# Kernel tuning notes

Measured on AMD Instinct MI355X. Metric: run time of the kernel, lower is better.

Reference implementation:

```python
import jax, jax.numpy as jnp
import numpy as np

E = 8192       # number of edges
D = 256        # edge feature dim


def setup_inputs() -> dict:
    key = jax.random.key(0)
    ks = jax.random.split(key, 4)
    s = 1.0 / np.sqrt(D)
    return {
        "edge_x": jax.random.normal(ks[0], (E, D), dtype=jnp.float32),
        "W_sim1": jax.random.normal(ks[1], (D, D), dtype=jnp.float32) * s,
        "b_sim1": jnp.zeros((D,), dtype=jnp.float32),
        "W_sim2": jax.random.normal(ks[2], (D, D), dtype=jnp.float32) * s,
        "b_sim2": jnp.zeros((D,), dtype=jnp.float32),
        "W_out": jax.random.normal(ks[3], (3 * D, D), dtype=jnp.float32) * (1.0 / np.sqrt(3 * D)),
        "b_out": jnp.zeros((D,), dtype=jnp.float32),
    }


def reference(edge_x, W_sim1, b_sim1, W_sim2, b_sim2, W_out, b_out):
    # MPModule.forward, 'fully' branch.
    # LinearBlock = Linear + ReLU (assumed).
    e1 = jax.nn.relu(edge_x @ W_sim1 + b_sim1)            # [E, D]
    # (e1.unsqueeze(1) * e1).mean(-1)  ==  (e1 @ e1.T) / D, avoiding [E,E,D]
    sim1 = (e1 @ e1.T) / D                                 # [E, E]
    e2 = jax.nn.relu(edge_x @ W_sim2 + b_sim2)             # [E, D]
    sim2 = (e2 @ e2.T) / D                                 # [E, E]
    # (edge_x * sim.unsqueeze(-1)).sum(1) == sim @ edge_x
    agg1 = sim1 @ edge_x                                   # [E, D]
    agg2 = sim2 @ edge_x                                   # [E, D]
    h = jnp.concatenate([edge_x, agg1, agg2], axis=-1)     # [E, 3D]
    return jax.nn.relu(h @ W_out + b_out)                  # [E, D]
```

## Files before the change

### kernel.cpp

```cpp
#include <hip/hip_runtime.h>
#include <hip/hip_bf16.h>


typedef short bf16x8  __attribute__((ext_vector_type(8)));
typedef short short4v __attribute__((ext_vector_type(4)));
typedef float f32x4   __attribute__((ext_vector_type(4)));

__device__ inline short f2bf(float x) {
    unsigned u = __builtin_bit_cast(unsigned, x);
    return (short)((u + 0x7fffu + ((u >> 16) & 1u)) >> 16);
}
__device__ inline float bf2f(short b) {
    return __builtin_bit_cast(float, (unsigned)((unsigned short)b) << 16);
}
__device__ inline void cp16_async(const char* g, char* l) {
    __builtin_amdgcn_global_load_lds(
        (const __attribute__((address_space(1))) unsigned int*)g,
        (__attribute__((address_space(3))) unsigned int*)l, 16, 0, 0);
}

__global__ void prep_all(const float* __restrict__ X, short* __restrict__ h,
                         int ldh, short* __restrict__ Xt,
                         const float* __restrict__ W1, const float* __restrict__ W2,
                         const float* __restrict__ Wo,
                         short* __restrict__ Wt1, short* __restrict__ Wt2,
                         short* __restrict__ Wtoh, short* __restrict__ Bt4,
                         float* __restrict__ M)
{
    __shared__ short tile[32][33];
    const int tx = threadIdx.x, ty = threadIdx.y;
    if (blockIdx.y < 8) {
        const int r0 = blockIdx.x * 32, c0 = blockIdx.y * 32;
        #pragma unroll
        for (int i = 0; i < 4; ++i) {
            int row = ty + i * 8;
            short b = f2bf(X[(size_t)(r0 + row) * 256 + c0 + tx]);
            tile[row][tx] = b;
            int slot = ((((c0 & 32) + tx) >> 3) ^ ((r0 + row) & 7));
            h[(size_t)(r0 + row) * ldh + (c0 & ~63) + slot * 8 + (tx & 7)] = b;
        }
        __syncthreads();
        #pragma unroll
        for (int i = 0; i < 4; ++i) {
            int row = ty + i * 8;
            int d = c0 + row;
            int slot = ((((r0 & 32) + tx) >> 3) ^ (d & 7));
            Xt[(size_t)d * 8192 + (r0 & ~63) + slot * 8 + (tx & 7)] = tile[tx][row];
        }
    } else {
        int tw = (blockIdx.y - 8) * 256 + blockIdx.x;
        if (tw >= 320) {
            int i0 = (tw - 320) * 256 + ty * 32 + tx;
            for (int i = i0; i < 131072; i += 49152) M[i] = 0.f;
            return;
        }
        const float* src; short* dst; int ldwt, dk0, kx, ny;
        if (tw < 64)       { src = W1; dst = Wt1; ldwt = 256;
                             kx = tw >> 3; ny = tw & 7; dk0 = kx * 32; }
        else if (tw < 128) { int u = tw - 64; src = W2; dst = Wt2; ldwt = 256;
                             kx = u >> 3; ny = u & 7; dk0 = kx * 32; }
        else               { int u = tw - 128; int g = u >> 6; int rem = u & 63;
                             kx = rem >> 3; ny = rem & 7;
                             src = Wo + (size_t)g * 256 * 256;
                             if (g == 0) { dst = Bt4;  ldwt = 768; dk0 = kx * 32; }
                             else        { dst = Wtoh; ldwt = 512;
                                           dk0 = (g - 1) * 256 + kx * 32; } }
        const int k0l = kx * 32, n0 = ny * 32;
        #pragma unroll
        for (int i = 0; i < 4; ++i) {
            int row = ty + i * 8;
            tile[row][tx] = f2bf(src[(size_t)(k0l + row) * 256 + n0 + tx]);
        }
        __syncthreads();
        #pragma unroll
        for (int i = 0; i < 4; ++i) {
            int row = ty + i * 8;
            int n = n0 + row;
            int slot = ((((dk0 & 32) + tx) >> 3) ^ (n & 7));
            dst[(size_t)n * ldwt + (dk0 & ~63) + slot * 8 + (tx & 7)] = tile[tx][row];
        }
    }
}

__global__ __launch_bounds__(256, 1)
void gemm128(const short* __restrict__ A0, const short* __restrict__ A1, int lda,
             const short* __restrict__ B0, const short* __restrict__ B1, int ldb,
             int K,
             const float* __restrict__ bias0, const float* __restrict__ bias1,
             void* __restrict__ out0, void* __restrict__ out1,
             short* __restrict__ hout, int ldh,
             int mode, float scale)
{
    int z = blockIdx.z, sim, kbeg, kend;
    if (mode == 2) { sim = z & 1; kbeg = (z >> 1) * 512; kend = kbeg + 512; }
    else           { sim = z;     kbeg = 0;              kend = K; }
    const short* Ap   = sim ? A1 : A0;
    const short* Bp   = sim ? B1 : B0;
    const float* bias = sim ? bias1 : bias0;

    const int m0 = blockIdx.x * 128, n0 = blockIdx.y * 128;
    const int t = threadIdx.x;
    const int w = t >> 6, l = t & 63, lr = l & 15, q = l >> 4;
    const int wm = w >> 1, wn = w & 1;
    const int wub = t & ~63;

    __shared__ __attribute__((aligned(16))) short S[2][2][128 * 64];

    f32x4 acc[4][4];
    #pragma unroll
    for (int i = 0; i < 4; ++i)
        #pragma unroll
        for (int j = 0; j < 4; ++j) acc[i][j] = f32x4{0.f, 0.f, 0.f, 0.f};

    auto stage = [&](int buf, int k0) {
        #pragma unroll
        for (int it = 0; it < 4; ++it) {
            int idx = it * 256 + t;
            int r = idx >> 3, s = idx & 7;
            cp16_async((const char*)(Ap + (size_t)(m0 + r) * lda + k0) + s * 16,
                       (char*)&S[buf][0][0] + (size_t)(it * 256 + wub) * 16);
        }
        #pragma unroll
        for (int it = 0; it < 4; ++it) {
            int idx = it * 256 + t;
            int r = idx >> 3, s = idx & 7;
            cp16_async((const char*)(Bp + (size_t)(n0 + r) * ldb + k0) + s * 16,
                       (char*)&S[buf][1][0] + (size_t)(it * 256 + wub) * 16);
        }
    };

    stage(0, kbeg);
    __syncthreads();
    int cur = 0;
    for (int k0 = kbeg; k0 < kend; k0 += 64) {
        if (k0 + 64 < kend) stage(cur ^ 1, k0 + 64);
        const short* As = &S[cur][0][0];
        const short* Bs = &S[cur][1][0];
        #pragma unroll
        for (int ks = 0; ks < 2; ++ks) {
            bf16x8 af[4], bfr[4];
            #pragma unroll
            for (int mt = 0; mt < 4; ++mt) {
                int ar = wm * 64 + mt * 16 + lr;
                af[mt] = *(const bf16x8*)&As[ar * 64 + (((ks*4 + q) ^ (ar & 7)) << 3)];
            }
            #pragma unroll
            for (int nt = 0; nt < 4; ++nt) {
                int br = wn * 64 + nt * 16 + lr;
                bfr[nt] = *(const bf16x8*)&Bs[br * 64 + (((ks*4 + q) ^ (br & 7)) << 3)];
            }
            #pragma unroll
            for (int mt = 0; mt < 4; ++mt)
                #pragma unroll
                for (int nt = 0; nt < 4; ++nt)
                    acc[mt][nt] = __builtin_amdgcn_mfma_f32_16x16x32_bf16(
                        af[mt], bfr[nt], acc[mt][nt], 0, 0, 0);
        }
        __syncthreads();
        cur ^= 1;
    }

    if (mode == 0) {
        #pragma unroll
        for (int mt = 0; mt < 4; ++mt)
            #pragma unroll
            for (int nt = 0; nt < 4; ++nt)
                #pragma unroll
                for (int r = 0; r < 4; ++r) {
                    int m = m0 + wm * 64 + mt * 16 + q * 4 + r;
                    int n = n0 + wn * 64 + nt * 16 + lr;
                    float v = acc[mt][nt][r] + bias[n];
                    ((float*)out0)[(size_t)m * 256 + n] = v > 0.f ? v : 0.f;
                }
    } else if (mode == 2) {
        float* Mo = (float*)out0 + (size_t)sim * 65536;
        #pragma unroll
        for (int mt = 0; mt < 4; ++mt)
            #pragma unroll
            for (int nt = 0; nt < 4; ++nt)
                #pragma unroll
                for (int r = 0; r < 4; ++r) {
                    int m = m0 + wm * 64 + mt * 16 + q * 4 + r;
                    int n = n0 + wn * 64 + nt * 16 + lr;
                    atomicAdd(&Mo[(size_t)m * 256 + n], acc[mt][nt][r] * scale);
                }
    } else {
        short* Hs = &S[0][0][0];
        short* Ts = &S[1][0][0];
        #pragma unroll
        for (int mt = 0; mt < 4; ++mt)
            #pragma unroll
            for (int nt = 0; nt < 4; ++nt) {
                int n_loc = wn * 64 + nt * 16 + lr;
                float bb = bias[n0 + n_loc];
                short vb[4];
                #pragma unroll
                for (int r = 0; r < 4; ++r) {
                    int m_loc = wm * 64 + mt * 16 + q * 4 + r;
                    float v = acc[mt][nt][r] + bb;
                    vb[r] = f2bf(v > 0.f ? v : 0.f);
                    Hs[m_loc * 128 + n_loc] = vb[r];
                }
                int gm = wm * 8 + mt * 2 + (q >> 1);
                short4v pk = { vb[0], vb[1], vb[2], vb[3] };
                *(short4v*)&Ts[n_loc * 128 + ((gm >> 3) << 6)
                               + (((gm & 7) ^ (n_loc & 7)) << 3) + ((q & 1) << 2)] = pk;
            }
        __syncthreads();
        short* et = (short*)(sim ? out1 : out0);
        const int cb = 256 + sim * 256 + n0;
        for (int i = t; i < 2048; i += 256) {
            int ml = i >> 4, g = i & 15;
            bf16x8 hv = *(const bf16x8*)&Hs[ml * 128 + g * 8];
            *(bf16x8*)(hout + (size_t)(m0 + ml) * ldh + cb + ((g >> 3) << 6)
                       + (((g & 7) ^ (ml & 7)) << 3)) = hv;
        }
        for (int i = t; i < 2048; i += 256) {
            int nl = i >> 4, s = i & 15;
            bf16x8 tv = *(const bf16x8*)&Ts[nl * 128 + s * 8];
            *(bf16x8*)(et + (size_t)(n0 + nl) * 8192 + m0 + s * 8) = tv;
        }
    }
}

__global__ __launch_bounds__(256, 1)
void gemm_small_n(const short* __restrict__ Wtoh, const float* __restrict__ M,
                  short* __restrict__ Bt4)
{
    const int sim = blockIdx.z;
    const int n0 = blockIdx.x * 64, c0 = blockIdx.y * 64;
    const int t = threadIdx.x;
    const int w = t >> 6, l = t & 63, lr = l & 15, q = l >> 4;
    const int wub = t & ~63;
    const float* Ms = M + (size_t)sim * 65536;

    __shared__ __attribute__((aligned(16))) short As[64 * 64];
    __shared__ __attribute__((aligned(16))) short Bs[64 * 64];

    f32x4 acc[4];
    #pragma unroll
    for (int i = 0; i < 4; ++i) acc[i] = f32x4{0.f, 0.f, 0.f, 0.f};

    for (int k0 = 0; k0 < 256; k0 += 64) {
        __syncthreads();
        #pragma unroll
        for (int it = 0; it < 2; ++it) {
            int idx = it * 256 + t;
            int r = idx >> 3, s = idx & 7;
            cp16_async((const char*)(Wtoh + (size_t)(n0 + r) * 512 + sim * 256 + k0) + s * 16,
                       (char*)As + (size_t)(it * 256 + wub) * 16);
        }
        for (int i = t; i < 512; i += 256) {
            int r = i >> 3, g = i & 7;
            const float* mp = Ms + (size_t)(c0 + r) * 256 + k0 + g * 8;
            f32x4 va = *(const f32x4*)mp;
            f32x4 vb = *(const f32x4*)(mp + 4);
            bf16x8 pk;
            pk[0] = f2bf(va[0]); pk[1] = f2bf(va[1]);
            pk[2] = f2bf(va[2]); pk[3] = f2bf(va[3]);
            pk[4] = f2bf(vb[0]); pk[5] = f2bf(vb[1]);
            pk[6] = f2bf(vb[2]); pk[7] = f2bf(vb[3]);
            *(bf16x8*)&Bs[r * 64 + ((g ^ (r & 7)) << 3)] = pk;
        }
        __syncthreads();
        #pragma unroll
        for (int ks = 0; ks < 2; ++ks) {
            int arow = w * 16 + lr;
            bf16x8 af = *(const bf16x8*)&As[arow * 64 + (((ks*4 + q) ^ (arow & 7)) << 3)];
            #pragma unroll
            for (int nt = 0; nt < 4; ++nt) {
                int brow = nt * 16 + lr;
                bf16x8 bfg = *(const bf16x8*)&Bs[brow * 64 + (((ks*4 + q) ^ (brow & 7)) << 3)];
                acc[nt] = __builtin_amdgcn_mfma_f32_16x16x32_bf16(af, bfg, acc[nt], 0, 0, 0);
            }
        }
    }
    __syncthreads();
    #pragma unroll
    for (int nt = 0; nt < 4; ++nt)
        #pragma unroll
        for (int r = 0; r < 4; ++r)
            As[(w * 16 + q * 4 + r) * 64 + nt * 16 + lr] = f2bf(acc[nt][r]);
    __syncthreads();
    const int cb = 256 + sim * 256 + c0;
    for (int i = t; i < 512; i += 256) {
        int rl = i >> 3, g = i & 7;
        bf16x8 v = *(const bf16x8*)&As[rl * 64 + g * 8];
        int m = n0 + rl;
        int slot = g ^ (m & 7);
        *(bf16x8*)(Bt4 + (size_t)m * 768 + cb + slot * 8) = v;
    }
}

extern "C" void kernel_launch(void* const* d_in, const int* in_sizes, int n_in,
                              void* d_out, int out_size, void* d_ws, size_t ws_size,
                              hipStream_t stream)
{
    const float* edge_x = (const float*)d_in[0];
    const float* W1 = (const float*)d_in[1];
    const float* b1 = (const float*)d_in[2];
    const float* W2 = (const float*)d_in[3];
    const float* b2 = (const float*)d_in[4];
    const float* Wo = (const float*)d_in[5];
    const float* bo = (const float*)d_in[6];

    char* ws = (char*)d_ws;
    short* h    = (short*)ws;
    short* Xt   = (short*)(ws + 12582912);
    short* e1t  = (short*)(ws + 16777216);
    short* e2t  = (short*)(ws + 20971520);
    short* Wt1  = (short*)(ws + 25165824);
    short* Wt2  = (short*)(ws + 25296896);
    short* Wtoh = (short*)(ws + 25427968);
    short* Bt4  = (short*)(ws + 25690112);
    float* M    = (float*)(ws + 26083328);

    prep_all<<<dim3(256, 10), dim3(32, 8), 0, stream>>>(
        edge_x, h, 768, Xt, W1, W2, Wo, Wt1, Wt2, Wtoh, Bt4, M);

    gemm128<<<dim3(64, 2, 2), 256, 0, stream>>>(
        h, h, 768, Wt1, Wt2, 256, 256, b1, b2, e1t, e2t, h, 768, 1, 0.f);

    gemm128<<<dim3(2, 2, 32), 256, 0, stream>>>(
        e1t, e2t, 8192, Xt, Xt, 8192, 8192, nullptr, nullptr, M, nullptr,
        nullptr, 0, 2, 1.0f / 256.0f);

    gemm_small_n<<<dim3(4, 4, 2), 256, 0, stream>>>(Wtoh, M, Bt4);

    gemm128<<<dim3(64, 2, 1), 256, 0, stream>>>(
        h, h, 768, Bt4, Bt4, 768, 768, bo, bo, (float*)d_out, nullptr,
        nullptr, 0, 0, 0.f);
}
```

Before: 115.1 us.

## Reassociate aggregation matmuls to precompute X@Wo slices, drop X transpose

Applies associativity so that agg_i @ Wo_i = (e_i^T (X Wo_i))^T-style products are built from G_i = X @ Wo_i, computed in the first GEMM launch alongside e1/e2. The split-K E-reduction now multiplies G_i^T by e_i instead of e_i^T by X, yielding Wo-projected 256x256 matrices directly. This removes the transposed-X write in prep and the separate small GEMM, which becomes a simple fp32-to-bf16 conversion. It adds work to the first launch (four z-slices instead of two) and changes the bf16 rounding order.

```diff
diff --git a/kernel.cpp b/kernel.cpp
--- a/kernel.cpp
+++ b/kernel.cpp
@@ -20,12 +20,11 @@
 }
 
 __global__ void prep_all(const float* __restrict__ X, short* __restrict__ h,
-                         int ldh, short* __restrict__ Xt,
                          const float* __restrict__ W1, const float* __restrict__ W2,
                          const float* __restrict__ Wo,
                          short* __restrict__ Wt1, short* __restrict__ Wt2,
-                         short* __restrict__ Wtoh, short* __restrict__ Bt4,
-                         float* __restrict__ M)
+                         short* __restrict__ Wto1, short* __restrict__ Wto2,
+                         short* __restrict__ Bt4, float* __restrict__ Nacc)
 {
     __shared__ short tile[32][33];
     const int tx = threadIdx.x, ty = threadIdx.y;
@@ -35,68 +34,75 @@
         for (int i = 0; i < 4; ++i) {
             int row = ty + i * 8;
             short b = f2bf(X[(size_t)(r0 + row) * 256 + c0 + tx]);
-            tile[row][tx] = b;
             int slot = ((((c0 & 32) + tx) >> 3) ^ ((r0 + row) & 7));
-            h[(size_t)(r0 + row) * ldh + (c0 & ~63) + slot * 8 + (tx & 7)] = b;
-        }
-        __syncthreads();
-        #pragma unroll
-        for (int i = 0; i < 4; ++i) {
-            int row = ty + i * 8;
-            int d = c0 + row;
-            int slot = ((((r0 & 32) + tx) >> 3) ^ (d & 7));
-            Xt[(size_t)d * 8192 + (r0 & ~63) + slot * 8 + (tx & 7)] = tile[tx][row];
-        }
+            h[(size_t)(r0 + row) * 768 + (c0 & ~63) + slot * 8 + (tx & 7)] = b;
+        }
+        return;
+    }
+    int tw = (blockIdx.y - 8) * 256 + blockIdx.x;
+    if (tw >= 320) {
+        int i0 = (tw - 320) * 256 + ty * 32 + tx;
+        for (int i = i0; i < 131072; i += 49152) Nacc[i] = 0.f;
+        return;
+    }
+    const float* src; short* dst; int ldwt, dk0, kx, ny;
+    if (tw < 64)       { src = W1; dst = Wt1; ldwt = 256;
+                         kx = tw >> 3; ny = tw & 7; dk0 = kx * 32; }
+    else if (tw < 128) { int u = tw - 64; src = W2; dst = Wt2; ldwt = 256;
+                         kx = u >> 3; ny = u & 7; dk0 = kx * 32; }
+    else               { int u = tw - 128; int g = u >> 6; int rem = u & 63;
+                         kx = rem >> 3; ny = rem & 7;
+                         src = Wo + (size_t)g * 65536;
+                         if (g == 0) { dst = Bt4; ldwt = 768; dk0 = kx * 32; }
+                         else        { dst = (g == 1) ? Wto1 : Wto2;
+                                       ldwt = 256; dk0 = kx * 32; } }
+    const int k0l = kx * 32, n0 = ny * 32;
+    #pragma unroll
+    for (int i = 0; i < 4; ++i) {
+        int row = ty + i * 8;
+        tile[row][tx] = f2bf(src[(size_t)(k0l + row) * 256 + n0 + tx]);
+    }
+    __syncthreads();
+    #pragma unroll
+    for (int i = 0; i < 4; ++i) {
+        int row = ty + i * 8;
+        int n = n0 + row;
+        int slot = ((((dk0 & 32) + tx) >> 3) ^ (n & 7));
+        dst[(size_t)n * ldwt + (dk0 & ~63) + slot * 8 + (tx & 7)] = tile[tx][row];
+    }
+}
+
+__global__ __launch_bounds__(256, 1)
+void gemm_all(int job, short* __restrict__ h,
+              const short* __restrict__ Wt1, const short* __restrict__ Wt2,
+              const short* __restrict__ Wto1, const short* __restrict__ Wto2,
+              const short* __restrict__ Bt4,
+              const float* __restrict__ b1, const float* __restrict__ b2,
+              const float* __restrict__ bo,
+              short* __restrict__ e1t, short* __restrict__ e2t,
+              short* __restrict__ G1t, short* __restrict__ G2t,
+              float* __restrict__ Nacc, float* __restrict__ outf)
+{
+    const int z = blockIdx.z;
+    int mode, sim = 0, kbeg = 0, kend, lda, ldb;
+    const short *Ap, *Bp;
+    const float* bias = nullptr;
+    short* et = nullptr;
+    if (job == 0) {
+        Ap = h; lda = 768; kend = 256; ldb = 256;
+        if (z < 2) { mode = 1; sim = z;     Bp = z ? Wt2 : Wt1;
+                     bias = z ? b2 : b1;    et = z ? e2t : e1t; }
+        else       { mode = 3; sim = z - 2; Bp = sim ? Wto2 : Wto1;
+                     et = sim ? G2t : G1t; }
+    } else if (job == 1) {
+        mode = 2; sim = z & 1;
+        kbeg = (z >> 1) * 512; kend = kbeg + 512;
+        Ap = sim ? G2t : G1t; lda = 8192;
+        Bp = sim ? e2t : e1t; ldb = 8192;
     } else {
-        int tw = (blockIdx.y - 8) * 256 + blockIdx.x;
-        if (tw >= 320) {
-            int i0 = (tw - 320) * 256 + ty * 32 + tx;
-            for (int i = i0; i < 131072; i += 49152) M[i] = 0.f;
-            return;
-        }
-        const float* src; short* dst; int ldwt, dk0, kx, ny;
-        if (tw < 64)       { src = W1; dst = Wt1; ldwt = 256;
-                             kx = tw >> 3; ny = tw & 7; dk0 = kx * 32; }
-        else if (tw < 128) { int u = tw - 64; src = W2; dst = Wt2; ldwt = 256;
-                             kx = u >> 3; ny = u & 7; dk0 = kx * 32; }
-        else               { int u = tw - 128; int g = u >> 6; int rem = u & 63;
-                             kx = rem >> 3; ny = rem & 7;
-                             src = Wo + (size_t)g * 256 * 256;
-                             if (g == 0) { dst = Bt4;  ldwt = 768; dk0 = kx * 32; }
-                             else        { dst = Wtoh; ldwt = 512;
-                                           dk0 = (g - 1) * 256 + kx * 32; } }
-        const int k0l = kx * 32, n0 = ny * 32;
-        #pragma unroll
-        for (int i = 0; i < 4; ++i) {
-            int row = ty + i * 8;
-            tile[row][tx] = f2bf(src[(size_t)(k0l + row) * 256 + n0 + tx]);
-        }
-        __syncthreads();
-        #pragma unroll
-        for (int i = 0; i < 4; ++i) {
-            int row = ty + i * 8;
-            int n = n0 + row;
-            int slot = ((((dk0 & 32) + tx) >> 3) ^ (n & 7));
-            dst[(size_t)n * ldwt + (dk0 & ~63) + slot * 8 + (tx & 7)] = tile[tx][row];
-        }
-    }
-}
-
-__global__ __launch_bounds__(256, 1)
-void gemm128(const short* __restrict__ A0, const short* __restrict__ A1, int lda,
-             const short* __restrict__ B0, const short* __restrict__ B1, int ldb,
-             int K,
-             const float* __restrict__ bias0, const float* __restrict__ bias1,
-             void* __restrict__ out0, void* __restrict__ out1,
-             short* __restrict__ hout, int ldh,
-             int mode, float scale)
-{
-    int z = blockIdx.z, sim, kbeg, kend;
-    if (mode == 2) { sim = z & 1; kbeg = (z >> 1) * 512; kend = kbeg + 512; }
-    else           { sim = z;     kbeg = 0;              kend = K; }
-    const short* Ap   = sim ? A1 : A0;
-    const short* Bp   = sim ? B1 : B0;
-    const float* bias = sim ? bias1 : bias0;
+        mode = 0; Ap = h; lda = 768; kend = 768;
+        Bp = Bt4; ldb = 768; bias = bo;
+    }
 
     const int m0 = blockIdx.x * 128, n0 = blockIdx.y * 128;
     const int t = threadIdx.x;
@@ -170,10 +176,10 @@
                     int m = m0 + wm * 64 + mt * 16 + q * 4 + r;
                     int n = n0 + wn * 64 + nt * 16 + lr;
                     float v = acc[mt][nt][r] + bias[n];
-                    ((float*)out0)[(size_t)m * 256 + n] = v > 0.f ? v : 0.f;
+                    outf[(size_t)m * 256 + n] = v > 0.f ? v : 0.f;
                 }
     } else if (mode == 2) {
-        float* Mo = (float*)out0 + (size_t)sim * 65536;
+        float* Mo = Nacc + (size_t)sim * 65536;
         #pragma unroll
         for (int mt = 0; mt < 4; ++mt)
             #pragma unroll
@@ -182,7 +188,8 @@
                 for (int r = 0; r < 4; ++r) {
                     int m = m0 + wm * 64 + mt * 16 + q * 4 + r;
                     int n = n0 + wn * 64 + nt * 16 + lr;
-                    atomicAdd(&Mo[(size_t)m * 256 + n], acc[mt][nt][r] * scale);
+                    atomicAdd(&Mo[(size_t)m * 256 + n],
+                              acc[mt][nt][r] * (1.0f / 256.0f));
                 }
     } else {
         short* Hs = &S[0][0][0];
@@ -192,14 +199,17 @@
             #pragma unroll
             for (int nt = 0; nt < 4; ++nt) {
                 int n_loc = wn * 64 + nt * 16 + lr;
-                float bb = bias[n0 + n_loc];
+                float bb = (mode == 1) ? bias[n0 + n_loc] : 0.f;
                 short vb[4];
                 #pragma unroll
                 for (int r = 0; r < 4; ++r) {
-                    int m_loc = wm * 64 + mt * 16 + q * 4 + r;
                     float v = acc[mt][nt][r] + bb;
-                    vb[r] = f2bf(v > 0.f ? v : 0.f);
-                    Hs[m_loc * 128 + n_loc] = vb[r];
+                    if (mode == 1) v = v > 0.f ? v : 0.f;
+                    vb[r] = f2bf(v);
+                    if (mode == 1) {
+                        int m_loc = wm * 64 + mt * 16 + q * 4 + r;
+                        Hs[m_loc * 128 + n_loc] = vb[r];
+                    }
                 }
                 int gm = wm * 8 + mt * 2 + (q >> 1);
                 short4v pk = { vb[0], vb[1], vb[2], vb[3] };
@@ -207,13 +217,14 @@
                                + (((gm & 7) ^ (n_loc & 7)) << 3) + ((q & 1) << 2)] = pk;
             }
         __syncthreads();
-        short* et = (short*)(sim ? out1 : out0);
-        const int cb = 256 + sim * 256 + n0;
-        for (int i = t; i < 2048; i += 256) {
-            int ml = i >> 4, g = i & 15;
-            bf16x8 hv = *(const bf16x8*)&Hs[ml * 128 + g * 8];
-            *(bf16x8*)(hout + (size_t)(m0 + ml) * ldh + cb + ((g >> 3) << 6)
-                       + (((g & 7) ^ (ml & 7)) << 3)) = hv;
+        if (mode == 1) {
+            const int cb = 256 + sim * 256 + n0;
+            for (int i = t; i < 2048; i += 256) {
+                int ml = i >> 4, g = i & 15;
+                bf16x8 hv = *(const bf16x8*)&Hs[ml * 128 + g * 8];
+                *(bf16x8*)(h + (size_t)(m0 + ml) * 768 + cb + ((g >> 3) << 6)
+                           + (((g & 7) ^ (ml & 7)) << 3)) = hv;
+            }
         }
         for (int i = t; i < 2048; i += 256) {
             int nl = i >> 4, s = i & 15;
@@ -223,73 +234,22 @@
     }
 }
 
-__global__ __launch_bounds__(256, 1)
-void gemm_small_n(const short* __restrict__ Wtoh, const float* __restrict__ M,
-                  short* __restrict__ Bt4)
-{
-    const int sim = blockIdx.z;
-    const int n0 = blockIdx.x * 64, c0 = blockIdx.y * 64;
-    const int t = threadIdx.x;
-    const int w = t >> 6, l = t & 63, lr = l & 15, q = l >> 4;
-    const int wub = t & ~63;
-    const float* Ms = M + (size_t)sim * 65536;
-
-    __shared__ __attribute__((aligned(16))) short As[64 * 64];
-    __shared__ __attribute__((aligned(16))) short Bs[64 * 64];
-
-    f32x4 acc[4];
-    #pragma unroll
-    for (int i = 0; i < 4; ++i) acc[i] = f32x4{0.f, 0.f, 0.f, 0.f};
-
-    for (int k0 = 0; k0 < 256; k0 += 64) {
-        __syncthreads();
-        #pragma unroll
-        for (int it = 0; it < 2; ++it) {
-            int idx = it * 256 + t;
-            int r = idx >> 3, s = idx & 7;
-            cp16_async((const char*)(Wtoh + (size_t)(n0 + r) * 512 + sim * 256 + k0) + s * 16,
-                       (char*)As + (size_t)(it * 256 + wub) * 16);
-        }
-        for (int i = t; i < 512; i += 256) {
-            int r = i >> 3, g = i & 7;
-            const float* mp = Ms + (size_t)(c0 + r) * 256 + k0 + g * 8;
-            f32x4 va = *(const f32x4*)mp;
-            f32x4 vb = *(const f32x4*)(mp + 4);
-            bf16x8 pk;
-            pk[0] = f2bf(va[0]); pk[1] = f2bf(va[1]);
-            pk[2] = f2bf(va[2]); pk[3] = f2bf(va[3]);
-            pk[4] = f2bf(vb[0]); pk[5] = f2bf(vb[1]);
-            pk[6] = f2bf(vb[2]); pk[7] = f2bf(vb[3]);
-            *(bf16x8*)&Bs[r * 64 + ((g ^ (r & 7)) << 3)] = pk;
-        }
-        __syncthreads();
-        #pragma unroll
-        for (int ks = 0; ks < 2; ++ks) {
-            int arow = w * 16 + lr;
-            bf16x8 af = *(const bf16x8*)&As[arow * 64 + (((ks*4 + q) ^ (arow & 7)) << 3)];
-            #pragma unroll
-            for (int nt = 0; nt < 4; ++nt) {
-                int brow = nt * 16 + lr;
-                bf16x8 bfg = *(const bf16x8*)&Bs[brow * 64 + (((ks*4 + q) ^ (brow & 7)) << 3)];
-                acc[nt] = __builtin_amdgcn_mfma_f32_16x16x32_bf16(af, bfg, acc[nt], 0, 0, 0);
-            }
-        }
-    }
-    __syncthreads();
-    #pragma unroll
-    for (int nt = 0; nt < 4; ++nt)
-        #pragma unroll
-        for (int r = 0; r < 4; ++r)
-            As[(w * 16 + q * 4 + r) * 64 + nt * 16 + lr] = f2bf(acc[nt][r]);
-    __syncthreads();
-    const int cb = 256 + sim * 256 + c0;
-    for (int i = t; i < 512; i += 256) {
-        int rl = i >> 3, g = i & 7;
-        bf16x8 v = *(const bf16x8*)&As[rl * 64 + g * 8];
-        int m = n0 + rl;
-        int slot = g ^ (m & 7);
-        *(bf16x8*)(Bt4 + (size_t)m * 768 + cb + slot * 8) = v;
-    }
+__global__ void convert_n(const float* __restrict__ Nacc, short* __restrict__ Bt4)
+{
+    int gid = blockIdx.x * 256 + threadIdx.x;
+    int sim = gid >> 13, rem = gid & 8191;
+    int n = rem >> 5, g = rem & 31;
+    const float* np = Nacc + (size_t)sim * 65536 + (size_t)n * 256 + g * 8;
+    f32x4 va = *(const f32x4*)np;
+    f32x4 vb = *(const f32x4*)(np + 4);
+    bf16x8 pk;
+    pk[0] = f2bf(va[0]); pk[1] = f2bf(va[1]);
+    pk[2] = f2bf(va[2]); pk[3] = f2bf(va[3]);
+    pk[4] = f2bf(vb[0]); pk[5] = f2bf(vb[1]);
+    pk[6] = f2bf(vb[2]); pk[7] = f2bf(vb[3]);
+    int k = 256 + sim * 256 + g * 8;
+    int slot = (g & 7) ^ (n & 7);
+    *(bf16x8*)(Bt4 + (size_t)n * 768 + (k & ~63) + slot * 8) = pk;
 }
 
 extern "C" void kernel_launch(void* const* d_in, const int* in_sizes, int n_in,
@@ -306,28 +266,33 @@
 
     char* ws = (char*)d_ws;
     short* h    = (short*)ws;
-    short* Xt   = (short*)(ws + 12582912);
-    short* e1t  = (short*)(ws + 16777216);
-    short* e2t  = (short*)(ws + 20971520);
-    short* Wt1  = (short*)(ws + 25165824);
-    short* Wt2  = (short*)(ws + 25296896);
-    short* Wtoh = (short*)(ws + 25427968);
-    short* Bt4  = (short*)(ws + 25690112);
-    float* M    = (float*)(ws + 26083328);
+    short* e1t  = (short*)(ws + 12582912);
+    short* e2t  = (short*)(ws + 16777216);
+    short* G1t  = (short*)(ws + 20971520);
+    short* G2t  = (short*)(ws + 25165824);
+    short* Wt1  = (short*)(ws + 29360128);
+    short* Wt2  = (short*)(ws + 29491200);
+    short* Wto1 = (short*)(ws + 29622272);
+    short* Wto2 = (short*)(ws + 29753344);
+    short* Bt4  = (short*)(ws + 29884416);
+    float* Nacc = (float*)(ws + 30277632);
+
+    float* out = (float*)d_out;
 
     prep_all<<<dim3(256, 10), dim3(32, 8), 0, stream>>>(
-        edge_x, h, 768, Xt, W1, W2, Wo, Wt1, Wt2, Wtoh, Bt4, M);
-
-    gemm128<<<dim3(64, 2, 2), 256, 0, stream>>>(
-        h, h, 768, Wt1, Wt2, 256, 256, b1, b2, e1t, e2t, h, 768, 1, 0.f);
-
-    gemm128<<<dim3(2, 2, 32), 256, 0, stream>>>(
-        e1t, e2t, 8192, Xt, Xt, 8192, 8192, nullptr, nullptr, M, nullptr,
-        nullptr, 0, 2, 1.0f / 256.0f);
-
-    gemm_small_n<<<dim3(4, 4, 2), 256, 0, stream>>>(Wtoh, M, Bt4);
-
-    gemm128<<<dim3(64, 2, 1), 256, 0, stream>>>(
-        h, h, 768, Bt4, Bt4, 768, 768, bo, bo, (float*)d_out, nullptr,
-        nullptr, 0, 0, 0.f);
-}
+        edge_x, h, W1, W2, Wo, Wt1, Wt2, Wto1, Wto2, Bt4, Nacc);
+
+    gemm_all<<<dim3(64, 2, 4), 256, 0, stream>>>(
+        0, h, Wt1, Wt2, Wto1, Wto2, Bt4, b1, b2, bo,
+        e1t, e2t, G1t, G2t, Nacc, out);
+
+    gemm_all<<<dim3(2, 2, 32), 256, 0, stream>>>(
+        1, h, Wt1, Wt2, Wto1, Wto2, Bt4, b1, b2, bo,
+        e1t, e2t, G1t, G2t, Nacc, out);
+
+    convert_n<<<dim3(64), 256, 0, stream>>>(Nacc, Bt4);
+
+    gemm_all<<<dim3(64, 2, 1), 256, 0, stream>>>(
+        2, h, Wt1, Wt2, Wto1, Wto2, Bt4, b1, b2, bo,
+        e1t, e2t, G1t, G2t, Nacc, out);
+}
```

Result: no change. 114.1 us (-0.9%).
